# Optimization experiments

Measured on AMD Instinct MI355X. Metric: run time of the kernel, lower is better.

The kernel has to match this reference:

```python
import jax, jax.numpy as jnp
import numpy as np

B, H, W, C_TOT = 8, 256, 256, 36
SIDX = slice(0, 3)    # special: Noll 1-3 -> 0-based 0..2
LIDX = slice(3, 6)    # low
MIDX = slice(6, 15)   # mid
HIDX = slice(15, 36)  # high


def _box3x3_sum(x):
    # x: [B, H, W]; 3x3 sliding-window sum with replicate (edge) padding.
    xp = jnp.pad(x, ((0, 0), (1, 1), (1, 1)), mode='edge')
    h, w = x.shape[1], x.shape[2]
    acc = jnp.zeros_like(x)
    for di in range(3):
        for dj in range(3):
            acc = acc + xp[:, di:di + h, dj:dj + w]
    return acc


def _group_core(z, bias, alpha, amax, eps, gss, p_sat):
    # z: [B, H, W, Cg]; all params shape [1]
    u = z + bias
    soft_abs = jnp.sqrt(u * u + eps)            # [B,H,W,Cg]
    s = _box3x3_sum(soft_abs.sum(axis=-1))      # [B,H,W] sum over channels and 3x3 window
    gain = gss / (1.0 + s / p_sat)              # [B,H,W]
    v = alpha * gain[..., None] * u
    return amax * jnp.tanh(v)


def setup_inputs() -> dict:
    key = jax.random.key(0)
    one = jnp.ones((1,), jnp.float32)
    inp = {
        'raw_coeffs': jax.random.normal(key, (B, H, W, C_TOT), dtype=jnp.float32),
        'special_bias': 0.0 * one, 'special_alpha': 1.0 * one,
        'special_amax': 1.0 * one, 'special_eps': 1e-6 * one,
        'low_bias': 0.0 * one, 'low_alpha': 1.0 * one, 'low_amax': 1.0 * one,
        'low_eps': 1e-6 * one, 'low_gss': 1.0 * one, 'low_p_sat': 1.0 * one,
        'mid_bias': 0.0 * one, 'mid_alpha': 1.0 * one, 'mid_amax': 1.0 * one,
        'mid_eps': 1e-6 * one, 'mid_gss': 1.0 * one, 'mid_p_sat': 1.0 * one,
        'high_bias': 0.0 * one, 'high_alpha': 1.0 * one, 'high_amax': 1.0 * one,
        'high_eps': 1e-6 * one, 'high_gss': 1.0 * one, 'high_p_sat': 1.0 * one,
    }
    return inp


def reference(raw_coeffs, special_bias, special_alpha, special_amax, special_eps,
              low_bias, low_alpha, low_amax, low_eps, low_gss, low_p_sat,
              mid_bias, mid_alpha, mid_amax, mid_eps, mid_gss, mid_p_sat,
              high_bias, high_alpha, high_amax, high_eps, high_gss, high_p_sat):
    # special group: plain affine + tanh (special_use_neighborhood=False)
    u_sp = raw_coeffs[..., SIDX] + special_bias
    out_sp = special_amax * jnp.tanh(special_alpha * u_sp)
    # local joint (3x3 coupled gain) groups
    out_lo = _group_core(raw_coeffs[..., LIDX], low_bias, low_alpha, low_amax, low_eps, low_gss, low_p_sat)
    out_mi = _group_core(raw_coeffs[..., MIDX], mid_bias, mid_alpha, mid_amax, mid_eps, mid_gss, mid_p_sat)
    out_hi = _group_core(raw_coeffs[..., HIDX], high_bias, high_alpha, high_amax, high_eps, high_gss, high_p_sat)
    return jnp.concatenate([out_sp, out_lo, out_mi, out_hi], axis=-1)
```

## Files before the change

kernel.cpp:

```cpp
#include <hip/hip_runtime.h>
#include <math.h>


static constexpr int IMG_H = 256;
static constexpr int IMG_W = 256;
static constexpr int NBATCH = 8;
static constexpr int CTOT = 36;
static constexpr int TS = 16;

__device__ __forceinline__ float fast_tanh(float x) {
    float e = __expf(2.0f * x);
    return 1.0f - __fdividef(2.0f, e + 1.0f);
}

__global__ __launch_bounds__(TS * TS) void lgz_kernel(
    const float* __restrict__ in, float* __restrict__ out,
    const float* __restrict__ p_sp_bias, const float* __restrict__ p_sp_alpha,
    const float* __restrict__ p_sp_amax,
    const float* __restrict__ p_lo_bias, const float* __restrict__ p_lo_alpha,
    const float* __restrict__ p_lo_amax, const float* __restrict__ p_lo_eps,
    const float* __restrict__ p_lo_gss, const float* __restrict__ p_lo_psat,
    const float* __restrict__ p_mi_bias, const float* __restrict__ p_mi_alpha,
    const float* __restrict__ p_mi_amax, const float* __restrict__ p_mi_eps,
    const float* __restrict__ p_mi_gss, const float* __restrict__ p_mi_psat,
    const float* __restrict__ p_hi_bias, const float* __restrict__ p_hi_alpha,
    const float* __restrict__ p_hi_amax, const float* __restrict__ p_hi_eps,
    const float* __restrict__ p_hi_gss, const float* __restrict__ p_hi_psat)
{
    __shared__ float s_lo[TS + 2][TS + 2];
    __shared__ float s_mi[TS + 2][TS + 2];
    __shared__ float s_hi[TS + 2][TS + 2];

    const int tx = threadIdx.x, ty = threadIdx.y;
    const int tid = ty * TS + tx;
    const int bx0 = blockIdx.x * TS, by0 = blockIdx.y * TS;
    const int b = blockIdx.z;

    const float b_sp = p_sp_bias[0], a_sp = p_sp_alpha[0], m_sp = p_sp_amax[0];
    const float b_lo = p_lo_bias[0], a_lo = p_lo_alpha[0], m_lo = p_lo_amax[0];
    const float e_lo = p_lo_eps[0],  g_lo = p_lo_gss[0],  q_lo = p_lo_psat[0];
    const float b_mi = p_mi_bias[0], a_mi = p_mi_alpha[0], m_mi = p_mi_amax[0];
    const float e_mi = p_mi_eps[0],  g_mi = p_mi_gss[0],  q_mi = p_mi_psat[0];
    const float b_hi = p_hi_bias[0], a_hi = p_hi_alpha[0], m_hi = p_hi_amax[0];
    const float e_hi = p_hi_eps[0],  g_hi = p_hi_gss[0],  q_hi = p_hi_psat[0];

    const float* img = in + (size_t)b * IMG_H * IMG_W * CTOT;
    const int gx = bx0 + tx, gy = by0 + ty;

    float v[CTOT];
    {
        const float4* p4 = reinterpret_cast<const float4*>(
            img + ((size_t)gy * IMG_W + gx) * CTOT);
        #pragma unroll
        for (int j = 0; j < 9; ++j) reinterpret_cast<float4*>(v)[j] = p4[j];
    }

    float tlo = 0.f, tmi = 0.f, thi = 0.f;
    #pragma unroll
    for (int c = 3; c < 6; ++c)   { float u = v[c] + b_lo; tlo += sqrtf(u * u + e_lo); }
    #pragma unroll
    for (int c = 6; c < 15; ++c)  { float u = v[c] + b_mi; tmi += sqrtf(u * u + e_mi); }
    #pragma unroll
    for (int c = 15; c < 36; ++c) { float u = v[c] + b_hi; thi += sqrtf(u * u + e_hi); }
    s_lo[ty + 1][tx + 1] = tlo;
    s_mi[ty + 1][tx + 1] = tmi;
    s_hi[ty + 1][tx + 1] = thi;

    if (tid < 4 * TS + 4) {
        int hy, hx;
        if (tid < TS + 2)                 { hy = 0;                         hx = tid; }
        else if (tid < 2 * (TS + 2))      { hy = TS + 1;                    hx = tid - (TS + 2); }
        else if (tid < 2 * (TS + 2) + TS) { hy = tid - 2 * (TS + 2) + 1;    hx = 0; }
        else                              { hy = tid - (2 * (TS + 2) + TS) + 1; hx = TS + 1; }
        const int gy2 = min(max(by0 + hy - 1, 0), IMG_H - 1);
        const int gx2 = min(max(bx0 + hx - 1, 0), IMG_W - 1);
        const float4* q4 = reinterpret_cast<const float4*>(
            img + ((size_t)gy2 * IMG_W + gx2) * CTOT);
        float w[CTOT];
        #pragma unroll
        for (int j = 0; j < 9; ++j) reinterpret_cast<float4*>(w)[j] = q4[j];
        float hlo = 0.f, hmi = 0.f, hhi = 0.f;
        #pragma unroll
        for (int c = 3; c < 6; ++c)   { float u = w[c] + b_lo; hlo += sqrtf(u * u + e_lo); }
        #pragma unroll
        for (int c = 6; c < 15; ++c)  { float u = w[c] + b_mi; hmi += sqrtf(u * u + e_mi); }
        #pragma unroll
        for (int c = 15; c < 36; ++c) { float u = w[c] + b_hi; hhi += sqrtf(u * u + e_hi); }
        s_lo[hy][hx] = hlo;
        s_mi[hy][hx] = hmi;
        s_hi[hy][hx] = hhi;
    }
    __syncthreads();

    float slo = 0.f, smi = 0.f, shi = 0.f;
    #pragma unroll
    for (int di = 0; di < 3; ++di) {
        #pragma unroll
        for (int dj = 0; dj < 3; ++dj) {
            slo += s_lo[ty + di][tx + dj];
            smi += s_mi[ty + di][tx + dj];
            shi += s_hi[ty + di][tx + dj];
        }
    }

    const float glo = a_lo * __fdividef(g_lo, 1.0f + __fdividef(slo, q_lo));
    const float gmi = a_mi * __fdividef(g_mi, 1.0f + __fdividef(smi, q_mi));
    const float ghi = a_hi * __fdividef(g_hi, 1.0f + __fdividef(shi, q_hi));

    float o[CTOT];
    #pragma unroll
    for (int c = 0; c < 3; ++c)   o[c] = m_sp * fast_tanh(a_sp * (v[c] + b_sp));
    #pragma unroll
    for (int c = 3; c < 6; ++c)   o[c] = m_lo * fast_tanh(glo * (v[c] + b_lo));
    #pragma unroll
    for (int c = 6; c < 15; ++c)  o[c] = m_mi * fast_tanh(gmi * (v[c] + b_mi));
    #pragma unroll
    for (int c = 15; c < 36; ++c) o[c] = m_hi * fast_tanh(ghi * (v[c] + b_hi));

    float4* o4 = reinterpret_cast<float4*>(
        out + ((size_t)gy * IMG_W + gx) * CTOT + (size_t)b * IMG_H * IMG_W * CTOT);
    #pragma unroll
    for (int j = 0; j < 9; ++j) o4[j] = reinterpret_cast<const float4*>(o)[j];
}

extern "C" void kernel_launch(void* const* d_in, const int* in_sizes, int n_in,
                              void* d_out, int out_size, void* d_ws, size_t ws_size,
                              hipStream_t stream) {
    const float* raw = (const float*)d_in[0];
    dim3 grid(IMG_W / TS, IMG_H / TS, NBATCH);
    dim3 block(TS, TS);
    lgz_kernel<<<grid, block, 0, stream>>>(
        raw, (float*)d_out,
        (const float*)d_in[1], (const float*)d_in[2], (const float*)d_in[3],
        (const float*)d_in[5], (const float*)d_in[6], (const float*)d_in[7],
        (const float*)d_in[8], (const float*)d_in[9], (const float*)d_in[10],
        (const float*)d_in[11], (const float*)d_in[12], (const float*)d_in[13],
        (const float*)d_in[14], (const float*)d_in[15], (const float*)d_in[16],
        (const float*)d_in[17], (const float*)d_in[18], (const float*)d_in[19],
        (const float*)d_in[20], (const float*)d_in[21], (const float*)d_in[22]);
}
```

Before: 46.45 us.

## Stage input tile with halo in LDS for coalesced loads and stores

The kernel now loads the whole 18x18x36 input tile, halo included, into shared memory using linear float4 indexing, so global reads are contiguous across threads. Halo pixels are read from shared memory instead of being fetched again from global. Results are written back into shared memory and then stored to global with a linear coalesced pattern. This targets the strided per-pixel 144-byte accesses of the old layout, at the cost of about 47KB of LDS per block, which lowers occupancy, plus an extra barrier.

```diff
diff --git a/kernel.cpp b/kernel.cpp
--- a/kernel.cpp
+++ b/kernel.cpp
@@ -2,18 +2,36 @@
 #include <math.h>
 
 
-static constexpr int IMG_H = 256;
-static constexpr int IMG_W = 256;
-static constexpr int NBATCH = 8;
-static constexpr int CTOT = 36;
+static constexpr int IMG = 256;
+static constexpr int NB = 8;
+static constexpr int C = 36;
 static constexpr int TS = 16;
+static constexpr int HT = TS + 2;
+static constexpr int ROWF4 = HT * 9;
+static constexpr int NSTAGE4 = HT * HT * 9;
+static constexpr int NOUT4 = TS * TS * 9;
 
 __device__ __forceinline__ float fast_tanh(float x) {
     float e = __expf(2.0f * x);
     return 1.0f - __fdividef(2.0f, e + 1.0f);
 }
 
-__global__ __launch_bounds__(TS * TS) void lgz_kernel(
+__device__ __forceinline__ void group_sums(const float* __restrict__ v,
+                                           float b_lo, float e_lo,
+                                           float b_mi, float e_mi,
+                                           float b_hi, float e_hi,
+                                           float& tlo, float& tmi, float& thi) {
+    float lo = 0.f, mi = 0.f, hi = 0.f;
+    #pragma unroll
+    for (int c = 3; c < 6; ++c)   { float u = v[c] + b_lo; lo += sqrtf(u * u + e_lo); }
+    #pragma unroll
+    for (int c = 6; c < 15; ++c)  { float u = v[c] + b_mi; mi += sqrtf(u * u + e_mi); }
+    #pragma unroll
+    for (int c = 15; c < 36; ++c) { float u = v[c] + b_hi; hi += sqrtf(u * u + e_hi); }
+    tlo = lo; tmi = mi; thi = hi;
+}
+
+__global__ __launch_bounds__(256) void lgz_kernel(
     const float* __restrict__ in, float* __restrict__ out,
     const float* __restrict__ p_sp_bias, const float* __restrict__ p_sp_alpha,
     const float* __restrict__ p_sp_amax,
@@ -27,12 +45,11 @@
     const float* __restrict__ p_hi_amax, const float* __restrict__ p_hi_eps,
     const float* __restrict__ p_hi_gss, const float* __restrict__ p_hi_psat)
 {
-    __shared__ float s_lo[TS + 2][TS + 2];
-    __shared__ float s_mi[TS + 2][TS + 2];
-    __shared__ float s_hi[TS + 2][TS + 2];
+    __shared__ __align__(16) float s_raw[HT * HT * C];
+    __shared__ float s_sum[3][HT][HT + 1];
 
-    const int tx = threadIdx.x, ty = threadIdx.y;
-    const int tid = ty * TS + tx;
+    const int tid = threadIdx.x;
+    const int tx = tid & 15, ty = tid >> 4;
     const int bx0 = blockIdx.x * TS, by0 = blockIdx.y * TS;
     const int b = blockIdx.z;
 
@@ -44,51 +61,56 @@
     const float b_hi = p_hi_bias[0], a_hi = p_hi_alpha[0], m_hi = p_hi_amax[0];
     const float e_hi = p_hi_eps[0],  g_hi = p_hi_gss[0],  q_hi = p_hi_psat[0];
 
-    const float* img = in + (size_t)b * IMG_H * IMG_W * CTOT;
-    const int gx = bx0 + tx, gy = by0 + ty;
+    const float* img = in + (size_t)b * IMG * IMG * C;
+    float* outimg = out + (size_t)b * IMG * IMG * C;
 
-    float v[CTOT];
+    #pragma unroll
+    for (int it = 0; it < (NSTAGE4 + 255) / 256; ++it) {
+        int F4 = tid + it * 256;
+        if (F4 < NSTAGE4) {
+            int r = F4 / ROWF4;
+            int rem = F4 - r * ROWF4;
+            int px = rem / 9;
+            int j = rem - px * 9;
+            int gy = min(max(by0 + r - 1, 0), IMG - 1);
+            int gx = min(max(bx0 + px - 1, 0), IMG - 1);
+            float4 val = *reinterpret_cast<const float4*>(
+                img + ((size_t)gy * IMG + gx) * C + j * 4);
+            *reinterpret_cast<float4*>(s_raw + (r * HT + px) * C + j * 4) = val;
+        }
+    }
+    __syncthreads();
+
+    float v[C];
     {
-        const float4* p4 = reinterpret_cast<const float4*>(
-            img + ((size_t)gy * IMG_W + gx) * CTOT);
+        const float* src = s_raw + ((ty + 1) * HT + (tx + 1)) * C;
         #pragma unroll
-        for (int j = 0; j < 9; ++j) reinterpret_cast<float4*>(v)[j] = p4[j];
+        for (int j = 0; j < 9; ++j)
+            reinterpret_cast<float4*>(v)[j] = reinterpret_cast<const float4*>(src)[j];
     }
-
-    float tlo = 0.f, tmi = 0.f, thi = 0.f;
-    #pragma unroll
-    for (int c = 3; c < 6; ++c)   { float u = v[c] + b_lo; tlo += sqrtf(u * u + e_lo); }
-    #pragma unroll
-    for (int c = 6; c < 15; ++c)  { float u = v[c] + b_mi; tmi += sqrtf(u * u + e_mi); }
-    #pragma unroll
-    for (int c = 15; c < 36; ++c) { float u = v[c] + b_hi; thi += sqrtf(u * u + e_hi); }
-    s_lo[ty + 1][tx + 1] = tlo;
-    s_mi[ty + 1][tx + 1] = tmi;
-    s_hi[ty + 1][tx + 1] = thi;
-
-    if (tid < 4 * TS + 4) {
+    {
+        float tlo, tmi, thi;
+        group_sums(v, b_lo, e_lo, b_mi, e_mi, b_hi, e_hi, tlo, tmi, thi);
+        s_sum[0][ty + 1][tx + 1] = tlo;
+        s_sum[1][ty + 1][tx + 1] = tmi;
+        s_sum[2][ty + 1][tx + 1] = thi;
+    }
+    if (tid < 68) {
         int hy, hx;
-        if (tid < TS + 2)                 { hy = 0;                         hx = tid; }
-        else if (tid < 2 * (TS + 2))      { hy = TS + 1;                    hx = tid - (TS + 2); }
-        else if (tid < 2 * (TS + 2) + TS) { hy = tid - 2 * (TS + 2) + 1;    hx = 0; }
-        else                              { hy = tid - (2 * (TS + 2) + TS) + 1; hx = TS + 1; }
-        const int gy2 = min(max(by0 + hy - 1, 0), IMG_H - 1);
-        const int gx2 = min(max(bx0 + hx - 1, 0), IMG_W - 1);
-        const float4* q4 = reinterpret_cast<const float4*>(
-            img + ((size_t)gy2 * IMG_W + gx2) * CTOT);
-        float w[CTOT];
+        if (tid < 18)      { hy = 0;            hx = tid; }
+        else if (tid < 36) { hy = HT - 1;       hx = tid - 18; }
+        else if (tid < 52) { hy = tid - 36 + 1; hx = 0; }
+        else               { hy = tid - 52 + 1; hx = HT - 1; }
+        float w[C];
+        const float* src = s_raw + (hy * HT + hx) * C;
         #pragma unroll
-        for (int j = 0; j < 9; ++j) reinterpret_cast<float4*>(w)[j] = q4[j];
-        float hlo = 0.f, hmi = 0.f, hhi = 0.f;
-        #pragma unroll
-        for (int c = 3; c < 6; ++c)   { float u = w[c] + b_lo; hlo += sqrtf(u * u + e_lo); }
-        #pragma unroll
-        for (int c = 6; c < 15; ++c)  { float u = w[c] + b_mi; hmi += sqrtf(u * u + e_mi); }
-        #pragma unroll
-        for (int c = 15; c < 36; ++c) { float u = w[c] + b_hi; hhi += sqrtf(u * u + e_hi); }
-        s_lo[hy][hx] = hlo;
-        s_mi[hy][hx] = hmi;
-        s_hi[hy][hx] = hhi;
+        for (int j = 0; j < 9; ++j)
+            reinterpret_cast<float4*>(w)[j] = reinterpret_cast<const float4*>(src)[j];
+        float tlo, tmi, thi;
+        group_sums(w, b_lo, e_lo, b_mi, e_mi, b_hi, e_hi, tlo, tmi, thi);
+        s_sum[0][hy][hx] = tlo;
+        s_sum[1][hy][hx] = tmi;
+        s_sum[2][hy][hx] = thi;
     }
     __syncthreads();
 
@@ -97,38 +119,51 @@
     for (int di = 0; di < 3; ++di) {
         #pragma unroll
         for (int dj = 0; dj < 3; ++dj) {
-            slo += s_lo[ty + di][tx + dj];
-            smi += s_mi[ty + di][tx + dj];
-            shi += s_hi[ty + di][tx + dj];
+            slo += s_sum[0][ty + di][tx + dj];
+            smi += s_sum[1][ty + di][tx + dj];
+            shi += s_sum[2][ty + di][tx + dj];
         }
     }
-
     const float glo = a_lo * __fdividef(g_lo, 1.0f + __fdividef(slo, q_lo));
     const float gmi = a_mi * __fdividef(g_mi, 1.0f + __fdividef(smi, q_mi));
     const float ghi = a_hi * __fdividef(g_hi, 1.0f + __fdividef(shi, q_hi));
 
-    float o[CTOT];
     #pragma unroll
-    for (int c = 0; c < 3; ++c)   o[c] = m_sp * fast_tanh(a_sp * (v[c] + b_sp));
+    for (int c = 0; c < 3; ++c)   v[c] = m_sp * fast_tanh(a_sp * (v[c] + b_sp));
     #pragma unroll
-    for (int c = 3; c < 6; ++c)   o[c] = m_lo * fast_tanh(glo * (v[c] + b_lo));
+    for (int c = 3; c < 6; ++c)   v[c] = m_lo * fast_tanh(glo * (v[c] + b_lo));
     #pragma unroll
-    for (int c = 6; c < 15; ++c)  o[c] = m_mi * fast_tanh(gmi * (v[c] + b_mi));
+    for (int c = 6; c < 15; ++c)  v[c] = m_mi * fast_tanh(gmi * (v[c] + b_mi));
     #pragma unroll
-    for (int c = 15; c < 36; ++c) o[c] = m_hi * fast_tanh(ghi * (v[c] + b_hi));
+    for (int c = 15; c < 36; ++c) v[c] = m_hi * fast_tanh(ghi * (v[c] + b_hi));
 
-    float4* o4 = reinterpret_cast<float4*>(
-        out + ((size_t)gy * IMG_W + gx) * CTOT + (size_t)b * IMG_H * IMG_W * CTOT);
+    {
+        float* dst = s_raw + ((ty + 1) * HT + (tx + 1)) * C;
+        #pragma unroll
+        for (int j = 0; j < 9; ++j)
+            reinterpret_cast<float4*>(dst)[j] = reinterpret_cast<const float4*>(v)[j];
+    }
+    __syncthreads();
+
     #pragma unroll
-    for (int j = 0; j < 9; ++j) o4[j] = reinterpret_cast<const float4*>(o)[j];
+    for (int it = 0; it < NOUT4 / 256; ++it) {
+        int F4 = tid + it * 256;
+        int p = F4 / 9;
+        int j = F4 - p * 9;
+        int r = p >> 4, cc = p & 15;
+        float4 val = *reinterpret_cast<const float4*>(
+            s_raw + ((r + 1) * HT + (cc + 1)) * C + 4 * j);
+        *reinterpret_cast<float4*>(
+            outimg + ((size_t)(by0 + r) * IMG + (bx0 + cc)) * C + 4 * j) = val;
+    }
 }
 
 extern "C" void kernel_launch(void* const* d_in, const int* in_sizes, int n_in,
                               void* d_out, int out_size, void* d_ws, size_t ws_size,
                               hipStream_t stream) {
     const float* raw = (const float*)d_in[0];
-    dim3 grid(IMG_W / TS, IMG_H / TS, NBATCH);
-    dim3 block(TS, TS);
+    dim3 grid(IMG / TS, IMG / TS, NB);
+    dim3 block(256);
     lgz_kernel<<<grid, block, 0, stream>>>(
         raw, (float*)d_out,
         (const float*)d_in[1], (const float*)d_in[2], (const float*)d_in[3],
```

New measurement: 47.24 us. No clear change (+1.7%).
